# Kernel optimization log

Measured on AMD Instinct MI355X. Metric: run time of the kernel, lower is better.

## Reference

```python
import jax, jax.numpy as jnp
import numpy as np

NUM_HEADS = 12
NUM_TASKS = 4


def setup_inputs() -> dict:
    key = jax.random.key(0)
    k1, k2, k3, k4 = jax.random.split(key, 4)
    B, N, C = 2, 2048, 768
    x = jax.random.normal(k1, (B, N, C), dtype=jnp.float32)
    # nn.Linear(dim, 3*dim, bias=False): store as [C, 3C] so y = x @ w_qkv
    w_qkv = jax.random.normal(k2, (C, 3 * C), dtype=jnp.float32) * (C ** -0.5)
    w_proj = jax.random.normal(k3, (C, C), dtype=jnp.float32) * (C ** -0.5)
    b_proj = jax.random.normal(k4, (C,), dtype=jnp.float32) * 0.01
    return {"x": x, "w_qkv": w_qkv, "w_proj": w_proj, "b_proj": b_proj}


def reference(x, w_qkv, w_proj, b_proj):
    B, N, C = x.shape
    H = NUM_HEADS
    d = C // H
    scale = d ** -0.5
    qkv = (x @ w_qkv).reshape(B, N, 3, H, d)
    qkv = jnp.transpose(qkv, (2, 0, 3, 1, 4))  # [3, B, H, N, d]
    q, k, v = qkv[0], qkv[1], qkv[2]
    attn = jnp.einsum("bhnd,bhmd->bhnm", q, k) * scale
    attn = jax.nn.softmax(attn, axis=-1)
    # static task mask: zero cross-task attention among first NUM_TASKS tokens
    mask = jnp.ones((N, N), dtype=attn.dtype).at[:NUM_TASKS, :NUM_TASKS].set(
        jnp.eye(NUM_TASKS, dtype=attn.dtype))
    attn = attn * mask  # broadcasts over [B, H, N, N]
    out = jnp.einsum("bhnm,bhmd->bhnd", attn, v)
    out = jnp.transpose(out, (0, 2, 1, 3)).reshape(B, N, C)
    return out @ w_proj + b_proj
```

## Files before the change

kernel.cpp:

```cpp
#include <hip/hip_runtime.h>

typedef __attribute__((ext_vector_type(4))) float f32x4;
typedef __attribute__((ext_vector_type(8))) __bf16 bf16x8;
typedef __attribute__((ext_vector_type(4))) __bf16 bf16x4;

#define QSCALE (0.125f * 1.4426950408889634f)

#define WAITV4 do { asm volatile("s_waitcnt vmcnt(4)" ::: "memory"); \
  __builtin_amdgcn_s_barrier(); __builtin_amdgcn_sched_barrier(0); } while (0)
#define WAITV0 do { asm volatile("s_waitcnt vmcnt(0)" ::: "memory"); \
  __builtin_amdgcn_s_barrier(); __builtin_amdgcn_sched_barrier(0); } while (0)

__device__ __forceinline__ void load_lds16(const void* g, void* l) {
  __builtin_amdgcn_global_load_lds(
      (const __attribute__((address_space(1))) unsigned int*)g,
      (__attribute__((address_space(3))) unsigned int*)l, 16, 0, 0);
}

__device__ __forceinline__ f32x4 mfma16(bf16x8 a, bf16x8 b, f32x4 c) {
  return __builtin_amdgcn_mfma_f32_16x16x32_bf16(a, b, c, 0, 0, 0);
}

__device__ __forceinline__ bf16x8 cat44(bf16x4 a, bf16x4 b) {
  return __builtin_shufflevector(a, b, 0, 1, 2, 3, 4, 5, 6, 7);
}


__global__ __launch_bounds__(256) void k_cast_x(const float* __restrict__ in,
                                                __bf16* __restrict__ out) {
  int i = blockIdx.x * 256 + threadIdx.x;
  const f32x4* in4 = (const f32x4*)in;
  f32x4 a = in4[i * 2], b = in4[i * 2 + 1];
  bf16x8 o;
  o[0] = (__bf16)a[0]; o[1] = (__bf16)a[1]; o[2] = (__bf16)a[2]; o[3] = (__bf16)a[3];
  o[4] = (__bf16)b[0]; o[5] = (__bf16)b[1]; o[6] = (__bf16)b[2]; o[7] = (__bf16)b[3];
  *(bf16x8*)(out + (size_t)i * 8) = o;
}

__global__ void k_transpose_cast2(const float* __restrict__ wqkv, __bf16* __restrict__ oq,
                                  const float* __restrict__ wproj, __bf16* __restrict__ op) {
  int z = blockIdx.z;
  if (z == 1 && blockIdx.x >= 24) return;
  const float* in = z ? wproj : wqkv;
  __bf16* out = z ? op : oq;
  int C = z ? 768 : 2304;
  __shared__ float t[32][33];
  int c0 = blockIdx.x * 32, r0 = blockIdx.y * 32;
  int tx = threadIdx.x, ty = threadIdx.y;
#pragma unroll
  for (int j = 0; j < 32; j += 8)
    t[ty + j][tx] = in[(size_t)(r0 + ty + j) * C + c0 + tx];
  __syncthreads();
#pragma unroll
  for (int j = 0; j < 32; j += 8)
    out[(size_t)(c0 + ty + j) * 768 + r0 + tx] = (__bf16)t[tx][ty + j];
}


__device__ __forceinline__ void gemm_core24(const char* aB, const char* bB,
                                            char* smem, int tid, int l,
                                            int wr, int wc, f32x4 (&acc)[4][4]) {
  auto stage = [&](int buf, int kt) {
#pragma unroll
    for (int is = 0; is < 2; ++is) {
      int o = is * 4096 + tid * 16;
      int row = o >> 6, cb = (o >> 4) & 3;
      int src = row * 1536 + (((cb ^ row) & 3) << 4) + kt * 64;
      load_lds16(aB + src, smem + buf * 8192 + o);
      load_lds16(bB + src, smem + 24576 + buf * 8192 + o);
    }
  };
  auto compute = [&](int buf) {
    const __bf16* As = (const __bf16*)(smem + buf * 8192);
    const __bf16* Bs = (const __bf16*)(smem + 24576 + buf * 8192);
    bf16x8 af[4], bfr[4];
#pragma unroll
    for (int mf = 0; mf < 4; ++mf) {
      int row = wr * 64 + mf * 16 + (l & 15);
      af[mf] = *(const bf16x8*)&As[row * 32 + ((((l >> 4) ^ row) & 3) << 3)];
    }
#pragma unroll
    for (int nf = 0; nf < 4; ++nf) {
      int row = wc * 64 + nf * 16 + (l & 15);
      bfr[nf] = *(const bf16x8*)&Bs[row * 32 + ((((l >> 4) ^ row) & 3) << 3)];
    }
    __builtin_amdgcn_s_setprio(1);
#pragma unroll
    for (int mf = 0; mf < 4; ++mf)
#pragma unroll
      for (int nf = 0; nf < 4; ++nf)
        acc[mf][nf] = mfma16(af[mf], bfr[nf], acc[mf][nf]);
    __builtin_amdgcn_s_setprio(0);
  };
  stage(0, 0); stage(1, 1);
#pragma unroll 3
  for (int t = 0; t < 21; ++t) {
    WAITV4;
    stage((t + 2) % 3, t + 2);
    compute(t % 3);
  }
  WAITV4; stage(2, 23); compute(0);
  WAITV4; compute(1);
  WAITV0; compute(2);
  __syncthreads();
}


__global__ __launch_bounds__(256, 3) void k_qkv(const __bf16* __restrict__ A,
                                                const __bf16* __restrict__ BT,
                                                __bf16* __restrict__ qb,
                                                __bf16* __restrict__ kb,
                                                __bf16* __restrict__ vT) {
  __shared__ __align__(16) char smem[49152];
  int tid = threadIdx.x, l = tid & 63, w = tid >> 6, wr = w >> 1, wc = w & 1;
  int g = l >> 4, c = l & 15;
  int m0 = blockIdx.y * 128, n0 = blockIdx.x * 128;
  f32x4 acc[4][4] = {};
  gemm_core24((const char*)(A + (size_t)m0 * 768), (const char*)(BT + (size_t)n0 * 768),
              smem, tid, l, wr, wc, acc);
  int b = m0 >> 11, m0l = m0 & 2047;
  int sel = n0 / 768;
  int rem = n0 - sel * 768;

  if (sel == 2) {
#pragma unroll
    for (int mf = 0; mf < 4; ++mf) {
      int tokb = wr * 64 + mf * 16 + 4 * g;
      int gr = tokb >> 3, low = (g & 1) << 3;
#pragma unroll
      for (int nf = 0; nf < 4; ++nf) {
        int dd = wc * 64 + nf * 16 + c;
        bf16x4 pk;
        pk[0] = (__bf16)acc[mf][nf][0]; pk[1] = (__bf16)acc[mf][nf][1];
        pk[2] = (__bf16)acc[mf][nf][2]; pk[3] = (__bf16)acc[mf][nf][3];
        *(bf16x4*)(smem + dd * 256 + (((gr ^ (dd & 15)) & 15) << 4) + low) = pk;
      }
    }
    __syncthreads();
#pragma unroll
    for (int p = 0; p < 8; ++p) {
      int idx = p * 256 + tid;
      int dd = idx >> 4, t8 = idx & 15;
      bf16x8 v = *(const bf16x8*)(smem + dd * 256 + (((t8 ^ (dd & 15)) & 15) << 4));
      int colg = rem + dd;
      int h = colg >> 6, d = colg & 63;
      *(bf16x8*)(vT + (((size_t)(b * 12 + h)) * 64 + d) * 2048 + m0l + t8 * 8) = v;
    }
  } else {
    float qs = (sel == 0) ? QSCALE : 1.0f;
#pragma unroll
    for (int mf = 0; mf < 4; ++mf)
#pragma unroll
      for (int nf = 0; nf < 4; ++nf) {
        int col = wc * 64 + nf * 16 + c;
        int grc = col >> 3, lowc = (col & 7) << 1;
#pragma unroll
        for (int r = 0; r < 4; ++r) {
          int tok = wr * 64 + mf * 16 + 4 * g + r;
          *(__bf16*)(smem + tok * 256 + (((grc ^ (tok & 15)) & 15) << 4) + lowc) =
              (__bf16)(acc[mf][nf][r] * qs);
        }
      }
    __syncthreads();
    __bf16* dst0 = (sel == 0) ? qb : kb;
#pragma unroll
    for (int p = 0; p < 8; ++p) {
      int idx = p * 256 + tid;
      int tok = idx >> 4, hh = (idx >> 3) & 1, d8 = idx & 7;
      int gr = hh * 8 + d8;
      bf16x8 v = *(const bf16x8*)(smem + tok * 256 + (((gr ^ (tok & 15)) & 15) << 4));
      int h = (rem >> 6) + hh;
      *(bf16x8*)(dst0 + (((size_t)(b * 12 + h)) * 2048 + m0l + tok) * 64 + d8 * 8) = v;
    }
  }
}


__global__ __launch_bounds__(256, 4) void k_attn(const __bf16* __restrict__ qb,
                                                 const __bf16* __restrict__ kb,
                                                 const __bf16* __restrict__ vT,
                                                 __bf16* __restrict__ Opart,
                                                 float* __restrict__ lpart) {
  __shared__ __align__(16) char smem[49152];
  int tid = threadIdx.x, l = tid & 63, w = tid >> 6;
  int g = l >> 4, c = l & 15;
  int phys = blockIdx.x;
  int lid = (phys & 7) * 96 + (phys >> 3);
  int qt = lid & 15;
  int bhsp = lid >> 4;
  int bh = bhsp % 24, sp = bhsp / 24;

  const char* qbase  = (const char*)qb + ((size_t)bh * 2048 + qt * 128) * 128;
  const char* kbase0 = (const char*)kb + (size_t)bh * 262144 + (size_t)sp * 131072;
  const char* vbase0 = (const char*)vT + (size_t)bh * 262144 + sp * 2048;

#pragma unroll
  for (int is = 0; is < 4; ++is) {
    int o = is * 4096 + tid * 16;
    int row = o >> 7, cb = (o >> 4) & 7;
    load_lds16(qbase + row * 128 + (((cb ^ row) & 7) << 4), smem + o);
  }
  __syncthreads();
  bf16x8 qf[2][2];
#pragma unroll
  for (int qi = 0; qi < 2; ++qi)
#pragma unroll
    for (int ks = 0; ks < 2; ++ks) {
      int q = w * 32 + qi * 16 + c;
      int gg = ks * 4 + g;
      qf[qi][ks] = *(const bf16x8*)(smem + q * 128 + (((gg ^ q) & 7) << 4));
    }
  __syncthreads();

  int low = (g & 1) << 3;
  int qkoff0 = c * 128 + (((g ^ c) & 7) << 4);
  int qkoff1 = c * 128 + ((((4 + g) ^ c) & 7) << 4);
  int vA0 = c * 128 + ((((g >> 1) ^ c) & 7) << 4) + low;
  int vB0 = c * 128 + ((((2 + (g >> 1)) ^ c) & 7) << 4) + low;
  int vA1 = c * 128 + ((((4 + (g >> 1)) ^ c) & 7) << 4) + low;
  int vB1 = c * 128 + ((((6 + (g >> 1)) ^ c) & 7) << 4) + low;

  auto stageKV = [&](int buf, int t) {
    const char* kbase = kbase0 + t * 8192;
    const char* vbase = vbase0 + t * 128;
#pragma unroll
    for (int is = 0; is < 2; ++is) {
      int o = is * 4096 + tid * 16;
      int r = o >> 7, cb = (o >> 4) & 7;
      load_lds16(kbase + r * 128 + (((cb ^ r) & 7) << 4), smem + buf * 8192 + o);
      load_lds16(vbase + (size_t)r * 4096 + (((cb ^ r) & 7) << 4),
                 smem + 24576 + buf * 8192 + o);
    }
  };

  f32x4 lacc4[2] = {};
  f32x4 accO[2][4] = {};

  auto compute = [&](int t, int buf) {
    const char* kq0 = smem + buf * 8192 + qkoff0;
    const char* kq1 = smem + buf * 8192 + qkoff1;
    const char* VsB = smem + 24576 + buf * 8192;
    const f32x4 z = {0.f, 0.f, 0.f, 0.f};
    f32x4 s[4][2];
    bf16x4 pkv[2][4];

    auto qk = [&](int kf) {
      bf16x8 k0 = *(const bf16x8*)(kq0 + kf * 2048);
      bf16x8 k1 = *(const bf16x8*)(kq1 + kf * 2048);
      __builtin_amdgcn_s_setprio(1);
      s[kf][0] = mfma16(k0, qf[0][0], z);
      s[kf][1] = mfma16(k0, qf[1][0], z);
      s[kf][0] = mfma16(k1, qf[0][1], s[kf][0]);
      s[kf][1] = mfma16(k1, qf[1][1], s[kf][1]);
      __builtin_amdgcn_s_setprio(0);
    };
    auto sm = [&](int kf) {
      f32x4 p0, p1;
#pragma unroll
      for (int r = 0; r < 4; ++r) {
        p0[r] = __builtin_amdgcn_exp2f(s[kf][0][r]);
        p1[r] = __builtin_amdgcn_exp2f(s[kf][1][r]);
      }
      if (kf == 0 && sp == 0 && qt == 0 && t == 0 && w == 0 && g == 0 && c < 4) {
#pragma unroll
        for (int r = 0; r < 4; ++r)
          if (r != c) p0[r] = 0.f;
      }
      lacc4[0] += p0;
      lacc4[1] += p1;
      bf16x4 a, b;
#pragma unroll
      for (int r = 0; r < 4; ++r) { a[r] = (__bf16)p0[r]; b[r] = (__bf16)p1[r]; }
      pkv[0][kf] = a;
      pkv[1][kf] = b;
    };
    auto pv = [&](int ks2) {
      bf16x8 pa0 = cat44(pkv[0][2 * ks2], pkv[0][2 * ks2 + 1]);
      bf16x8 pa1 = cat44(pkv[1][2 * ks2], pkv[1][2 * ks2 + 1]);
      const char* p0 = VsB + (ks2 ? vA1 : vA0);
      const char* p1 = VsB + (ks2 ? vB1 : vB0);
      __builtin_amdgcn_s_setprio(1);
#pragma unroll
      for (int df = 0; df < 4; ++df) {
        bf16x4 v0 = *(const bf16x4*)(p0 + df * 2048);
        bf16x4 v1 = *(const bf16x4*)(p1 + df * 2048);
        bf16x8 vb = cat44(v0, v1);
        accO[0][df] = mfma16(pa0, vb, accO[0][df]);
        accO[1][df] = mfma16(pa1, vb, accO[1][df]);
      }
      __builtin_amdgcn_s_setprio(0);
    };

    qk(0); qk(1);
    sm(0);
    qk(2);
    sm(1);
    pv(0);
    qk(3);
    sm(2);
    sm(3);
    pv(1);
  };

  stageKV(0, 0); stageKV(1, 1);
#pragma unroll 3
  for (int t = 0; t < 12; ++t) {
    WAITV4;
    stageKV((t + 2) % 3, t + 2);
    compute(t, t % 3);
  }
  WAITV4; stageKV(2, 14); compute(12, 0);
  WAITV4; stageKV(0, 15); compute(13, 1);
  WAITV4; compute(14, 2);
  WAITV0; compute(15, 0);
  __syncthreads();

  size_t pbase = ((size_t)sp * 24 + bh) * 2048 + qt * 128;
  float lfull[2];
#pragma unroll
  for (int qi = 0; qi < 2; ++qi) {
    float rr = lacc4[qi][0] + lacc4[qi][1] + lacc4[qi][2] + lacc4[qi][3];
    rr += __shfl_xor(rr, 16, 64);
    rr += __shfl_xor(rr, 32, 64);
    lfull[qi] = rr;
  }
  if (g == 0) {
#pragma unroll
    for (int qi = 0; qi < 2; ++qi)
      lpart[pbase + w * 32 + qi * 16 + c] = lfull[qi];
  }

  char* ep = smem + w * 4096;
#pragma unroll
  for (int mf = 0; mf < 2; ++mf) {
#pragma unroll
    for (int df = 0; df < 4; ++df) {
      int col = df * 16 + c;
      int sI = col >> 2, lowc = (col & 3) << 2;
#pragma unroll
      for (int r = 0; r < 4; ++r) {
        int rloc = 4 * g + r;
        *(float*)(ep + rloc * 256 + (((sI ^ rloc) & 15) << 4) + lowc) = accO[mf][df][r];
      }
    }
    asm volatile("s_waitcnt lgkmcnt(0)" ::: "memory");
    int rr = l >> 2, q4 = l & 3;
    f32x4 aa[4];
#pragma unroll
    for (int j = 0; j < 4; ++j) {
      int sj = q4 * 4 + j;
      aa[j] = *(const f32x4*)(ep + rr * 256 + (((sj ^ rr) & 15) << 4));
    }
    bf16x8 o0, o1;
#pragma unroll
    for (int j = 0; j < 4; ++j) { o0[j] = (__bf16)aa[0][j]; o0[4 + j] = (__bf16)aa[1][j]; }
#pragma unroll
    for (int j = 0; j < 4; ++j) { o1[j] = (__bf16)aa[2][j]; o1[4 + j] = (__bf16)aa[3][j]; }
    int q = w * 32 + mf * 16 + rr;
    char* dst = (char*)Opart + (pbase + q) * 128 + q4 * 32;
    *(bf16x8*)dst = o0;
    *(bf16x8*)(dst + 16) = o1;
  }
}


__global__ __launch_bounds__(256) void k_combine(const __bf16* __restrict__ Opart,
                                                 const float* __restrict__ lpart,
                                                 __bf16* __restrict__ ao) {
  int i = blockIdx.x * 256 + threadIdx.x;
  int d8 = i & 7, q = (i >> 3) & 2047, bh = i >> 14;
  int bg = bh / 12, h = bh - bg * 12;
  const size_t SPL = 24ull * 2048 * 64;
  size_t o0 = (((size_t)bh) * 2048 + q) * 64 + d8 * 8;
  bf16x8 a = *(const bf16x8*)(Opart + o0);
  bf16x8 b = *(const bf16x8*)(Opart + SPL + o0);
  size_t lq = (size_t)bh * 2048 + q;
  float lsum = lpart[lq] + lpart[24ull * 2048 + lq];
  float rl = __builtin_amdgcn_rcpf(lsum);
  bf16x8 o;
#pragma unroll
  for (int j = 0; j < 8; ++j)
    o[j] = (__bf16)(((float)a[j] + (float)b[j]) * rl);
  *(bf16x8*)(ao + ((size_t)bg * 2048 + q) * 768 + h * 64 + d8 * 8) = o;
}


__global__ __launch_bounds__(256, 3) void k_proj(const __bf16* __restrict__ A,
                                                 const __bf16* __restrict__ BT,
                                                 const float* __restrict__ bias,
                                                 float* __restrict__ out) {
  __shared__ __align__(16) char smem[49152];
  int tid = threadIdx.x, l = tid & 63, w = tid >> 6, wr = w >> 1, wc = w & 1;
  int m0 = blockIdx.y * 128, n0 = blockIdx.x * 128;
  f32x4 acc[4][4] = {};
  gemm_core24((const char*)(A + (size_t)m0 * 768), (const char*)(BT + (size_t)n0 * 768),
              smem, tid, l, wr, wc, acc);
#pragma unroll
  for (int nf = 0; nf < 4; ++nf) {
    int cc = n0 + wc * 64 + nf * 16 + (l & 15);
    float bi = bias[cc];
#pragma unroll
    for (int mf = 0; mf < 4; ++mf) {
      int m = m0 + wr * 64 + mf * 16 + ((l >> 4) << 2);
#pragma unroll
      for (int r = 0; r < 4; ++r)
        out[(size_t)(m + r) * 768 + cc] = acc[mf][nf][r] + bi;
    }
  }
}


extern "C" void kernel_launch(void* const* d_in, const int* in_sizes, int n_in,
                              void* d_out, int out_size, void* d_ws, size_t ws_size,
                              hipStream_t stream) {
  const float* x      = (const float*)d_in[0];
  const float* w_qkv  = (const float*)d_in[1];
  const float* w_proj = (const float*)d_in[2];
  const float* b_proj = (const float*)d_in[3];
  float* out = (float*)d_out;

  char* ws = (char*)d_ws;
  size_t off = 0;
  auto alloc = [&](size_t bytes) {
    char* p = ws + off;
    off += (bytes + 255) & ~(size_t)255;
    return p;
  };
  __bf16* xb     = (__bf16*)alloc(4096ull * 768 * 2);
  __bf16* wqkvT  = (__bf16*)alloc(2304ull * 768 * 2);
  __bf16* wprojT = (__bf16*)alloc(768ull * 768 * 2);
  __bf16* qb     = (__bf16*)alloc(24ull * 2048 * 64 * 2);
  __bf16* kb     = (__bf16*)alloc(24ull * 2048 * 64 * 2);
  __bf16* vT     = (__bf16*)alloc(24ull * 64 * 2048 * 2);
  __bf16* ao     = (__bf16*)alloc(4096ull * 768 * 2);
  __bf16* Opart  = (__bf16*)alloc(2ull * 24 * 2048 * 64 * 2);
  float*  lpart  = (float*)alloc(2ull * 24 * 2048 * 4);

  k_cast_x<<<1536, 256, 0, stream>>>(x, xb);
  k_transpose_cast2<<<dim3(72, 24, 2), dim3(32, 8), 0, stream>>>(w_qkv, wqkvT, w_proj, wprojT);
  k_qkv<<<dim3(18, 32), 256, 0, stream>>>(xb, wqkvT, qb, kb, vT);
  k_attn<<<768, 256, 0, stream>>>(qb, kb, vT, Opart, lpart);
  k_combine<<<1536, 256, 0, stream>>>(Opart, lpart, ao);
  k_proj<<<dim3(6, 32), 256, 0, stream>>>(ao, wprojT, b_proj, out);
}
```

Before: 91.41 us.

## Fuse split-KV combine into projection GEMM and compute row sums via MFMA

The separate combine kernel is removed. The projection GEMM now reads both split-KV partial outputs and partial sums directly, normalizes them in registers and writes bf16 A tiles into LDS, double-buffered against async B loads. In the attention kernel the softmax denominator is accumulated with an extra MFMA against a ones vector, replacing the VALU adds and cross-lane shuffles. This saves one launch and the round trip of the ao buffer through memory. In exchange the GEMM A path becomes register-staged and is recomputed for each of the 6 column blocks, and the row sums now come from bf16-rounded probabilities.

```diff
diff --git a/kernel.cpp b/kernel.cpp
--- a/kernel.cpp
+++ b/kernel.cpp
@@ -220,6 +220,10 @@
   int vA1 = c * 128 + ((((4 + (g >> 1)) ^ c) & 7) << 4) + low;
   int vB1 = c * 128 + ((((6 + (g >> 1)) ^ c) & 7) << 4) + low;
 
+  bf16x8 ones8;
+#pragma unroll
+  for (int j = 0; j < 8; ++j) ones8[j] = (__bf16)1.0f;
+
   auto stageKV = [&](int buf, int t) {
     const char* kbase = kbase0 + t * 8192;
     const char* vbase = vbase0 + t * 128;
@@ -233,7 +237,7 @@
     }
   };
 
-  f32x4 lacc4[2] = {};
+  f32x4 accL[2] = {};
   f32x4 accO[2][4] = {};
 
   auto compute = [&](int t, int buf) {
@@ -266,8 +270,6 @@
         for (int r = 0; r < 4; ++r)
           if (r != c) p0[r] = 0.f;
       }
-      lacc4[0] += p0;
-      lacc4[1] += p1;
       bf16x4 a, b;
 #pragma unroll
       for (int r = 0; r < 4; ++r) { a[r] = (__bf16)p0[r]; b[r] = (__bf16)p1[r]; }
@@ -288,6 +290,8 @@
         accO[0][df] = mfma16(pa0, vb, accO[0][df]);
         accO[1][df] = mfma16(pa1, vb, accO[1][df]);
       }
+      accL[0] = mfma16(pa0, ones8, accL[0]);
+      accL[1] = mfma16(pa1, ones8, accL[1]);
       __builtin_amdgcn_s_setprio(0);
     };
 
@@ -316,18 +320,12 @@
   __syncthreads();
 
   size_t pbase = ((size_t)sp * 24 + bh) * 2048 + qt * 128;
-  float lfull[2];
-#pragma unroll
-  for (int qi = 0; qi < 2; ++qi) {
-    float rr = lacc4[qi][0] + lacc4[qi][1] + lacc4[qi][2] + lacc4[qi][3];
-    rr += __shfl_xor(rr, 16, 64);
-    rr += __shfl_xor(rr, 32, 64);
-    lfull[qi] = rr;
-  }
-  if (g == 0) {
+  if (c == 0) {
 #pragma unroll
     for (int qi = 0; qi < 2; ++qi)
-      lpart[pbase + w * 32 + qi * 16 + c] = lfull[qi];
+#pragma unroll
+      for (int r = 0; r < 4; ++r)
+        lpart[pbase + w * 32 + qi * 16 + 4 * g + r] = accL[qi][r];
   }
 
   char* ep = smem + w * 4096;
@@ -364,37 +362,97 @@
 }
 
 
-__global__ __launch_bounds__(256) void k_combine(const __bf16* __restrict__ Opart,
-                                                 const float* __restrict__ lpart,
-                                                 __bf16* __restrict__ ao) {
-  int i = blockIdx.x * 256 + threadIdx.x;
-  int d8 = i & 7, q = (i >> 3) & 2047, bh = i >> 14;
-  int bg = bh / 12, h = bh - bg * 12;
-  const size_t SPL = 24ull * 2048 * 64;
-  size_t o0 = (((size_t)bh) * 2048 + q) * 64 + d8 * 8;
-  bf16x8 a = *(const bf16x8*)(Opart + o0);
-  bf16x8 b = *(const bf16x8*)(Opart + SPL + o0);
-  size_t lq = (size_t)bh * 2048 + q;
-  float lsum = lpart[lq] + lpart[24ull * 2048 + lq];
-  float rl = __builtin_amdgcn_rcpf(lsum);
-  bf16x8 o;
-#pragma unroll
-  for (int j = 0; j < 8; ++j)
-    o[j] = (__bf16)(((float)a[j] + (float)b[j]) * rl);
-  *(bf16x8*)(ao + ((size_t)bg * 2048 + q) * 768 + h * 64 + d8 * 8) = o;
-}
-
-
-__global__ __launch_bounds__(256, 3) void k_proj(const __bf16* __restrict__ A,
-                                                 const __bf16* __restrict__ BT,
-                                                 const float* __restrict__ bias,
-                                                 float* __restrict__ out) {
-  __shared__ __align__(16) char smem[49152];
+__global__ __launch_bounds__(256, 4) void k_projf(const __bf16* __restrict__ Opart,
+                                                  const float* __restrict__ lpart,
+                                                  const __bf16* __restrict__ BT,
+                                                  const float* __restrict__ bias,
+                                                  float* __restrict__ out) {
+  __shared__ __align__(16) char smem[32768];
   int tid = threadIdx.x, l = tid & 63, w = tid >> 6, wr = w >> 1, wc = w & 1;
   int m0 = blockIdx.y * 128, n0 = blockIdx.x * 128;
+  const char* bB = (const char*)(BT + (size_t)n0 * 768);
+  int bg = m0 >> 11, m0l = m0 & 2047;
+  const size_t SPL = 24ull * 2048 * 64;
+  const size_t LPL = 24ull * 2048;
+
+  int row0 = tid >> 2;
+  int cb = tid & 3;
+
+  auto stageB = [&](int buf, int kt) {
+#pragma unroll
+    for (int is = 0; is < 2; ++is) {
+      int o = is * 4096 + tid * 16;
+      int r = o >> 6, c2 = (o >> 4) & 3;
+      int src = r * 1536 + (((c2 ^ r) & 3) << 4) + kt * 64;
+      load_lds16(bB + src, smem + 16384 + buf * 8192 + o);
+    }
+  };
+
+  bf16x8 aR0[2], aR1[2];
+  float lsR[2];
+  auto loadA = [&](int kt) {
+    int h = kt >> 1;
+#pragma unroll
+    for (int is = 0; is < 2; ++is) {
+      int row = row0 + is * 64;
+      int ch = (cb ^ row) & 3;
+      int tok = m0l + row;
+      size_t lq = (size_t)(bg * 12 + h) * 2048 + tok;
+      size_t base = lq * 64 + (kt & 1) * 32 + ch * 8;
+      aR0[is] = *(const bf16x8*)(Opart + base);
+      aR1[is] = *(const bf16x8*)(Opart + SPL + base);
+      lsR[is] = lpart[lq] + lpart[LPL + lq];
+    }
+  };
+  auto writeA = [&](int buf) {
+#pragma unroll
+    for (int is = 0; is < 2; ++is) {
+      float rl = __builtin_amdgcn_rcpf(lsR[is]);
+      bf16x8 o8;
+#pragma unroll
+      for (int j = 0; j < 8; ++j)
+        o8[j] = (__bf16)(((float)aR0[is][j] + (float)aR1[is][j]) * rl);
+      *(bf16x8*)(smem + buf * 8192 + is * 4096 + tid * 16) = o8;
+    }
+  };
+
   f32x4 acc[4][4] = {};
-  gemm_core24((const char*)(A + (size_t)m0 * 768), (const char*)(BT + (size_t)n0 * 768),
-              smem, tid, l, wr, wc, acc);
+  auto compute = [&](int buf) {
+    const __bf16* As = (const __bf16*)(smem + buf * 8192);
+    const __bf16* Bs = (const __bf16*)(smem + 16384 + buf * 8192);
+    bf16x8 af[4], bfr[4];
+#pragma unroll
+    for (int mf = 0; mf < 4; ++mf) {
+      int row = wr * 64 + mf * 16 + (l & 15);
+      af[mf] = *(const bf16x8*)&As[row * 32 + ((((l >> 4) ^ row) & 3) << 3)];
+    }
+#pragma unroll
+    for (int nf = 0; nf < 4; ++nf) {
+      int row = wc * 64 + nf * 16 + (l & 15);
+      bfr[nf] = *(const bf16x8*)&Bs[row * 32 + ((((l >> 4) ^ row) & 3) << 3)];
+    }
+    __builtin_amdgcn_s_setprio(1);
+#pragma unroll
+    for (int mf = 0; mf < 4; ++mf)
+#pragma unroll
+      for (int nf = 0; nf < 4; ++nf)
+        acc[mf][nf] = mfma16(af[mf], bfr[nf], acc[mf][nf]);
+    __builtin_amdgcn_s_setprio(0);
+  };
+
+  stageB(0, 0);
+  loadA(0);
+  writeA(0);
+  __syncthreads();
+#pragma unroll 2
+  for (int kt = 0; kt < 24; ++kt) {
+    int cur = kt & 1;
+    if (kt + 1 < 24) { stageB(cur ^ 1, kt + 1); loadA(kt + 1); }
+    compute(cur);
+    if (kt + 1 < 24) writeA(cur ^ 1);
+    __syncthreads();
+  }
+
 #pragma unroll
   for (int nf = 0; nf < 4; ++nf) {
     int cc = n0 + wc * 64 + nf * 16 + (l & 15);
@@ -432,7 +490,6 @@
   __bf16* qb     = (__bf16*)alloc(24ull * 2048 * 64 * 2);
   __bf16* kb     = (__bf16*)alloc(24ull * 2048 * 64 * 2);
   __bf16* vT     = (__bf16*)alloc(24ull * 64 * 2048 * 2);
-  __bf16* ao     = (__bf16*)alloc(4096ull * 768 * 2);
   __bf16* Opart  = (__bf16*)alloc(2ull * 24 * 2048 * 64 * 2);
   float*  lpart  = (float*)alloc(2ull * 24 * 2048 * 4);
 
@@ -440,6 +497,5 @@
   k_transpose_cast2<<<dim3(72, 24, 2), dim3(32, 8), 0, stream>>>(w_qkv, wqkvT, w_proj, wprojT);
   k_qkv<<<dim3(18, 32), 256, 0, stream>>>(xb, wqkvT, qb, kb, vT);
   k_attn<<<768, 256, 0, stream>>>(qb, kb, vT, Opart, lpart);
-  k_combine<<<1536, 256, 0, stream>>>(Opart, lpart, ao);
-  k_proj<<<dim3(6, 32), 256, 0, stream>>>(ao, wprojT, b_proj, out);
-}
+  k_projf<<<dim3(6, 32), 256, 0, stream>>>(Opart, lpart, wprojT, b_proj, out);
+}
```

After: 109.2 us. 1.19x slower.

## Split K/V staging with double-buffered V and compute row sums via MFMA

Applied to the files above, without the earlier changes.

Staging of K and V tiles is decoupled: K keeps a triple buffer while V is double-buffered and prefetched only one step ahead, which shrinks shared memory from 48KB to 40KB and may let more blocks fit per CU. The softmax denominator is no longer built with per-lane vector adds and cross-lane shuffles. It is now accumulated by extra MFMAs of P against a ones vector, and each row sum is written directly from the accumulator layout. This trades two extra MFMAs per PV step, and a shorter prefetch distance for V, for fewer VALU ops and less LDS use.

```diff
diff --git a/kernel.cpp b/kernel.cpp
--- a/kernel.cpp
+++ b/kernel.cpp
@@ -7,6 +7,8 @@
 #define QSCALE (0.125f * 1.4426950408889634f)
 
 #define WAITV4 do { asm volatile("s_waitcnt vmcnt(4)" ::: "memory"); \
+  __builtin_amdgcn_s_barrier(); __builtin_amdgcn_sched_barrier(0); } while (0)
+#define WAITV2 do { asm volatile("s_waitcnt vmcnt(2)" ::: "memory"); \
   __builtin_amdgcn_s_barrier(); __builtin_amdgcn_sched_barrier(0); } while (0)
 #define WAITV0 do { asm volatile("s_waitcnt vmcnt(0)" ::: "memory"); \
   __builtin_amdgcn_s_barrier(); __builtin_amdgcn_sched_barrier(0); } while (0)
@@ -181,7 +183,7 @@
                                                  const __bf16* __restrict__ vT,
                                                  __bf16* __restrict__ Opart,
                                                  float* __restrict__ lpart) {
-  __shared__ __align__(16) char smem[49152];
+  __shared__ __align__(16) char smem[40960];
   int tid = threadIdx.x, l = tid & 63, w = tid >> 6;
   int g = l >> 4, c = l & 15;
   int phys = blockIdx.x;
@@ -220,26 +222,37 @@
   int vA1 = c * 128 + ((((4 + (g >> 1)) ^ c) & 7) << 4) + low;
   int vB1 = c * 128 + ((((6 + (g >> 1)) ^ c) & 7) << 4) + low;
 
-  auto stageKV = [&](int buf, int t) {
+  bf16x8 ones8;
+#pragma unroll
+  for (int j = 0; j < 8; ++j) ones8[j] = (__bf16)1.0f;
+
+  auto stageK = [&](int buf, int t) {
     const char* kbase = kbase0 + t * 8192;
-    const char* vbase = vbase0 + t * 128;
 #pragma unroll
     for (int is = 0; is < 2; ++is) {
       int o = is * 4096 + tid * 16;
       int r = o >> 7, cb = (o >> 4) & 7;
       load_lds16(kbase + r * 128 + (((cb ^ r) & 7) << 4), smem + buf * 8192 + o);
+    }
+  };
+  auto stageV = [&](int buf, int t) {
+    const char* vbase = vbase0 + t * 128;
+#pragma unroll
+    for (int is = 0; is < 2; ++is) {
+      int o = is * 4096 + tid * 16;
+      int r = o >> 7, cb = (o >> 4) & 7;
       load_lds16(vbase + (size_t)r * 4096 + (((cb ^ r) & 7) << 4),
                  smem + 24576 + buf * 8192 + o);
     }
   };
 
-  f32x4 lacc4[2] = {};
+  f32x4 accL[2] = {};
   f32x4 accO[2][4] = {};
 
-  auto compute = [&](int t, int buf) {
-    const char* kq0 = smem + buf * 8192 + qkoff0;
-    const char* kq1 = smem + buf * 8192 + qkoff1;
-    const char* VsB = smem + 24576 + buf * 8192;
+  auto compute = [&](int t, int kbuf, int vbuf) {
+    const char* kq0 = smem + kbuf * 8192 + qkoff0;
+    const char* kq1 = smem + kbuf * 8192 + qkoff1;
+    const char* VsB = smem + 24576 + vbuf * 8192;
     const f32x4 z = {0.f, 0.f, 0.f, 0.f};
     f32x4 s[4][2];
     bf16x4 pkv[2][4];
@@ -266,8 +279,6 @@
         for (int r = 0; r < 4; ++r)
           if (r != c) p0[r] = 0.f;
       }
-      lacc4[0] += p0;
-      lacc4[1] += p1;
       bf16x4 a, b;
 #pragma unroll
       for (int r = 0; r < 4; ++r) { a[r] = (__bf16)p0[r]; b[r] = (__bf16)p1[r]; }
@@ -288,6 +299,8 @@
         accO[0][df] = mfma16(pa0, vb, accO[0][df]);
         accO[1][df] = mfma16(pa1, vb, accO[1][df]);
       }
+      accL[0] = mfma16(pa0, ones8, accL[0]);
+      accL[1] = mfma16(pa1, ones8, accL[1]);
       __builtin_amdgcn_s_setprio(0);
     };
 
@@ -302,32 +315,24 @@
     pv(1);
   };
 
-  stageKV(0, 0); stageKV(1, 1);
-#pragma unroll 3
-  for (int t = 0; t < 12; ++t) {
-    WAITV4;
-    stageKV((t + 2) % 3, t + 2);
-    compute(t, t % 3);
-  }
-  WAITV4; stageKV(2, 14); compute(12, 0);
-  WAITV4; stageKV(0, 15); compute(13, 1);
-  WAITV4; compute(14, 2);
-  WAITV0; compute(15, 0);
+  stageK(0, 0); stageV(0, 0); stageK(1, 1);
+  for (int t = 0; t < 14; ++t) {
+    WAITV2;
+    stageV((t + 1) & 1, t + 1);
+    stageK((t + 2) % 3, t + 2);
+    compute(t, t % 3, t & 1);
+  }
+  WAITV2; stageV(1, 15); compute(14, 2, 0);
+  WAITV0; compute(15, 0, 1);
   __syncthreads();
 
   size_t pbase = ((size_t)sp * 24 + bh) * 2048 + qt * 128;
-  float lfull[2];
-#pragma unroll
-  for (int qi = 0; qi < 2; ++qi) {
-    float rr = lacc4[qi][0] + lacc4[qi][1] + lacc4[qi][2] + lacc4[qi][3];
-    rr += __shfl_xor(rr, 16, 64);
-    rr += __shfl_xor(rr, 32, 64);
-    lfull[qi] = rr;
-  }
-  if (g == 0) {
+  if (c == 0) {
 #pragma unroll
     for (int qi = 0; qi < 2; ++qi)
-      lpart[pbase + w * 32 + qi * 16 + c] = lfull[qi];
+#pragma unroll
+      for (int r = 0; r < 4; ++r)
+        lpart[pbase + w * 32 + qi * 16 + 4 * g + r] = accL[qi][r];
   }
 
   char* ep = smem + w * 4096;
```

Result: faster. 88.89 us (-2.8%).
